# Performance work log

Measured on AMD Instinct MI355X. Metric: run time of the kernel, lower is better.

## Reference

```python
import jax, jax.numpy as jnp
import numpy as np

N, M = 8192, 4096
SCALE = 1e-4  # keeps tss ~ O(1) so the gaussian score doesn't underflow


def setup_inputs() -> dict:
    key = jax.random.key(0)
    x = jax.random.normal(key, (N, M), dtype=jnp.float32) * SCALE
    variance = jnp.asarray(0.9, dtype=jnp.float32)
    return {"x": x, "variance": variance}


def reference(x, variance):
    # _lpd vectorized over all columns at once.
    # series_a/series_b are first differences with a leading zero row; the
    # leading zeros contribute 0 to the sum (0*0>=0 -> 0-0), so we can work
    # directly on the diffs.
    d = jnp.diff(x, axis=0)                 # [N-1, M]
    da = d[:, :1]                           # reference column diffs [N-1, 1]
    db = d[:, 1:]                           # other column diffs    [N-1, M-1]
    diff = da - db
    hpdd = jnp.where(da * db >= 0, diff, jnp.abs(diff))
    tss = jnp.sum(hpdd, axis=0)             # [M-1]
    # torch.tensor(self.tss) detaches tss from x's autograd graph
    tss = jax.lax.stop_gradient(tss)

    # gaussian score with mean 0, sigma = variance
    sqrt_2pi = jnp.sqrt(jnp.asarray(2.0 * np.pi, dtype=x.dtype))
    coef = 1.0 / (sqrt_2pi * variance)
    score = coef * jnp.exp(-(tss ** 2) / (2.0 * variance ** 2))  # [M-1]

    # tan-softmax weighting
    t = jnp.tan(score)
    w = t / jnp.sum(t)                      # [M-1]

    y = jnp.reshape(jnp.sum(w * x[:, 1:]), (-1,))  # [1]
    return y
```

## Files before the change

kernel.cpp:

```cpp
#include <hip/hip_runtime.h>
#include <math.h>

#define NROWS 8192
#define NCOLS 4096
#define RPC 16
#define NCHUNK (NROWS / RPC)
#define TPB 1024
#define CPT 4
#define F2BLK 64
#define TPB2 512
#define CPB2 (NCOLS / F2BLK)
#define PARTS 8

typedef float f32x4 __attribute__((ext_vector_type(4)));

__global__ __launch_bounds__(TPB, 8) void tss_partial_kernel(
    const float* __restrict__ x,
    float* __restrict__ ptss,
    float* __restrict__ pcs)
{
    const int tid   = threadIdx.x;
    const int chunk = blockIdx.x;
    const int col   = tid * CPT;
    const int r0    = chunk * RPC;

    __shared__ float x0[RPC + 1];
    __shared__ float da_sh[RPC];

    if (tid <= RPC) {
        int r = min(r0 + tid, NROWS - 1);
        x0[tid] = x[(size_t)r * NCOLS];
    }
    __syncthreads();
    if (tid < RPC) {
        da_sh[tid] = (r0 + tid + 1 < NROWS) ? (x0[tid + 1] - x0[tid]) : 0.0f;
    }
    __syncthreads();

    const f32x4* row = (const f32x4*)(x + (size_t)r0 * NCOLS + col);
    const int rs = NCOLS / 4;
    const int maxoff = NROWS - 1 - r0;

    float tss0 = 0.f, tss1 = 0.f, tss2 = 0.f, tss3 = 0.f;
    float cs0 = 0.f, cs1 = 0.f, cs2 = 0.f, cs3 = 0.f;

    f32x4 cur = row[0];
    f32x4 nxt = row[min(1, maxoff) * rs];

    #pragma unroll 4
    for (int i = 0; i < RPC; ++i) {
        const int offc = (i + 2 <= RPC) ? (i + 2) : RPC;
        const int off  = min(offc, maxoff);
        f32x4 pf = row[off * rs];

        cs0 += cur.x; cs1 += cur.y; cs2 += cur.z; cs3 += cur.w;

        const float da = da_sh[i];
        float db, df;
        db = nxt.x - cur.x; df = da - db;
        tss0 += (da * db >= 0.f) ? df : fabsf(df);
        db = nxt.y - cur.y; df = da - db;
        tss1 += (da * db >= 0.f) ? df : fabsf(df);
        db = nxt.z - cur.z; df = da - db;
        tss2 += (da * db >= 0.f) ? df : fabsf(df);
        db = nxt.w - cur.w; df = da - db;
        tss3 += (da * db >= 0.f) ? df : fabsf(df);

        cur = nxt;
        nxt = pf;
    }

    float* pt = ptss + (size_t)chunk * NCOLS + col;
    float* pc = pcs  + (size_t)chunk * NCOLS + col;
    *(f32x4*)pt = (f32x4){tss0, tss1, tss2, tss3};
    *(f32x4*)pc = (f32x4){cs0, cs1, cs2, cs3};
}

__global__ __launch_bounds__(TPB2) void tss_finalize_kernel(
    const float* __restrict__ ptss,
    const float* __restrict__ pcs,
    const float* __restrict__ variance,
    double* __restrict__ blk)
{
    const int tid  = threadIdx.x;
    const int part = tid >> 6;
    const int cpos = tid & 63;
    const int j    = blockIdx.x * CPB2 + cpos;

    double tss = 0.0, cs = 0.0;
    #pragma unroll 8
    for (int c = part * (NCHUNK / PARTS); c < (part + 1) * (NCHUNK / PARTS); ++c) {
        tss += (double)ptss[(size_t)c * NCOLS + j];
        cs  += (double)pcs[(size_t)c * NCOLS + j];
    }

    __shared__ double stss[PARTS][CPB2];
    __shared__ double scs[PARTS][CPB2];
    stss[part][cpos] = tss;
    scs[part][cpos]  = cs;
    __syncthreads();

    if (tid < CPB2) {
        tss = 0.0; cs = 0.0;
        #pragma unroll
        for (int p = 0; p < PARTS; ++p) { tss += stss[p][tid]; cs += scs[p][tid]; }

        double t = 0.0, tc = 0.0;
        const int jj = blockIdx.x * CPB2 + tid;
        if (jj >= 1) {
            const double var = (double)variance[0];
            const double SQRT_2PI = 2.5066282746310005024;
            const double coef = 1.0 / (SQRT_2PI * var);
            const double score = coef * exp(-(tss * tss) / (2.0 * var * var));
            t  = tan(score);
            tc = t * cs;
        }
        for (int o = 32; o > 0; o >>= 1) {
            t  += __shfl_down(t, o);
            tc += __shfl_down(tc, o);
        }
        if (tid == 0) {
            blk[2 * blockIdx.x]     = t;
            blk[2 * blockIdx.x + 1] = tc;
        }
    }
}

__global__ __launch_bounds__(64) void tss_reduce_kernel(
    const double* __restrict__ blk,
    float* __restrict__ out)
{
    const int tid = threadIdx.x;
    double st  = blk[2 * tid];
    double stc = blk[2 * tid + 1];
    for (int o = 32; o > 0; o >>= 1) {
        st  += __shfl_down(st, o);
        stc += __shfl_down(stc, o);
    }
    if (tid == 0) out[0] = (float)(stc / st);
}

extern "C" void kernel_launch(void* const* d_in, const int* in_sizes, int n_in,
                              void* d_out, int out_size, void* d_ws, size_t ws_size,
                              hipStream_t stream) {
    const float* x   = (const float*)d_in[0];
    const float* var = (const float*)d_in[1];
    float* out = (float*)d_out;

    float* ptss = (float*)d_ws;
    float* pcs  = ptss + (size_t)NCHUNK * NCOLS;
    double* blk = (double*)(pcs + (size_t)NCHUNK * NCOLS);

    tss_partial_kernel<<<NCHUNK, TPB, 0, stream>>>(x, ptss, pcs);
    tss_finalize_kernel<<<F2BLK, TPB2, 0, stream>>>(ptss, pcs, var, blk);
    tss_reduce_kernel<<<1, 64, 0, stream>>>(blk, out);
}
```

Before: 38.92 us.

## Halve partial-sum chunks and widen finalize reduction across more blocks

Doubles the rows each partial block handles, so half as many blocks run and half as many per-chunk tss and column-sum partials are written to and re-read from workspace. The finalize kernel moves from 64 blocks of 512 threads to 256 blocks of 1024 threads. Each block now owns 16 columns split over 64 chunk ranges and combines them with a shared-memory tree reduction. The aim is to cut intermediate memory traffic and spread the finalize work over more CUs. The cost is fewer, longer partial blocks, narrower 64-byte column reads in finalize, and a run of __syncthreads steps in the tree reduction.

```diff
diff --git a/kernel.cpp b/kernel.cpp
--- a/kernel.cpp
+++ b/kernel.cpp
@@ -3,18 +3,18 @@
 
 #define NROWS 8192
 #define NCOLS 4096
-#define RPC 16
+#define RPC 32
 #define NCHUNK (NROWS / RPC)
 #define TPB 1024
 #define CPT 4
-#define F2BLK 64
-#define TPB2 512
+#define F2BLK 256
+#define TPB2 1024
 #define CPB2 (NCOLS / F2BLK)
-#define PARTS 8
+#define PARTS2 64
 
 typedef float f32x4 __attribute__((ext_vector_type(4)));
 
-__global__ __launch_bounds__(TPB, 8) void tss_partial_kernel(
+__global__ __launch_bounds__(TPB) void tss_partial_kernel(
     const float* __restrict__ x,
     float* __restrict__ ptss,
     float* __restrict__ pcs)
@@ -47,7 +47,7 @@
     f32x4 cur = row[0];
     f32x4 nxt = row[min(1, maxoff) * rs];
 
-    #pragma unroll 4
+    #pragma unroll 8
     for (int i = 0; i < RPC; ++i) {
         const int offc = (i + 2 <= RPC) ? (i + 2) : RPC;
         const int off  = min(offc, maxoff);
@@ -83,27 +83,36 @@
     double* __restrict__ blk)
 {
     const int tid  = threadIdx.x;
-    const int part = tid >> 6;
-    const int cpos = tid & 63;
-    const int j    = blockIdx.x * CPB2 + cpos;
+    const int cg   = tid & 15;
+    const int part = tid >> 4;
+    const int j    = blockIdx.x * CPB2 + cg;
 
     double tss = 0.0, cs = 0.0;
-    #pragma unroll 8
-    for (int c = part * (NCHUNK / PARTS); c < (part + 1) * (NCHUNK / PARTS); ++c) {
+    const int c0 = part * (NCHUNK / PARTS2);
+    #pragma unroll
+    for (int k = 0; k < NCHUNK / PARTS2; ++k) {
+        const int c = c0 + k;
         tss += (double)ptss[(size_t)c * NCOLS + j];
         cs  += (double)pcs[(size_t)c * NCOLS + j];
     }
 
-    __shared__ double stss[PARTS][CPB2];
-    __shared__ double scs[PARTS][CPB2];
-    stss[part][cpos] = tss;
-    scs[part][cpos]  = cs;
+    __shared__ double stss[PARTS2][CPB2 + 1];
+    __shared__ double scs[PARTS2][CPB2 + 1];
+    stss[part][cg] = tss;
+    scs[part][cg]  = cs;
     __syncthreads();
 
+    for (int s = PARTS2 / 2; s >= 1; s >>= 1) {
+        if (part < s) {
+            stss[part][cg] += stss[part + s][cg];
+            scs[part][cg]  += scs[part + s][cg];
+        }
+        __syncthreads();
+    }
+
     if (tid < CPB2) {
-        tss = 0.0; cs = 0.0;
-        #pragma unroll
-        for (int p = 0; p < PARTS; ++p) { tss += stss[p][tid]; cs += scs[p][tid]; }
+        const double tssT = stss[0][tid];
+        const double csT  = scs[0][tid];
 
         double t = 0.0, tc = 0.0;
         const int jj = blockIdx.x * CPB2 + tid;
@@ -111,11 +120,11 @@
             const double var = (double)variance[0];
             const double SQRT_2PI = 2.5066282746310005024;
             const double coef = 1.0 / (SQRT_2PI * var);
-            const double score = coef * exp(-(tss * tss) / (2.0 * var * var));
+            const double score = coef * exp(-(tssT * tssT) / (2.0 * var * var));
             t  = tan(score);
-            tc = t * cs;
+            tc = t * csT;
         }
-        for (int o = 32; o > 0; o >>= 1) {
+        for (int o = 8; o > 0; o >>= 1) {
             t  += __shfl_down(t, o);
             tc += __shfl_down(tc, o);
         }
@@ -131,8 +140,12 @@
     float* __restrict__ out)
 {
     const int tid = threadIdx.x;
-    double st  = blk[2 * tid];
-    double stc = blk[2 * tid + 1];
+    double st = 0.0, stc = 0.0;
+    #pragma unroll
+    for (int k = 0; k < F2BLK / 64; ++k) {
+        st  += blk[2 * (tid + 64 * k)];
+        stc += blk[2 * (tid + 64 * k) + 1];
+    }
     for (int o = 32; o > 0; o >>= 1) {
         st  += __shfl_down(st, o);
         stc += __shfl_down(stc, o);
```

After: 33.04 us. 1.18x faster.
